# Kernel tuning notes

Measured on AMD Instinct MI355X. Metric: run time of the kernel, lower is better.

## Reference

```python
import jax, jax.numpy as jnp
import numpy as np

B, N, E, IN = 16, 4096, 65536, 128
FILTERS = [256, 256, 128]


def setup_inputs() -> dict:
    key = jax.random.key(0)
    ks = jax.random.split(key, 12)
    inp = {
        "x": jax.random.normal(ks[0], (B, N, IN), dtype=jnp.float32),
        "edge_index": jax.random.randint(ks[1], (B, 2, E), 0, N, dtype=jnp.int32),
        "edge_weight": jax.random.uniform(ks[2], (B, E), dtype=jnp.float32),
        "mask": jax.random.randint(ks[3], (B, N), 0, 2, dtype=jnp.int32),
    }
    dims = [IN] + FILTERS
    for i in range(3):
        inp[f"W{i+1}"] = jax.random.normal(ks[4 + 2 * i], (dims[i], dims[i + 1]), dtype=jnp.float32) / np.sqrt(dims[i]).astype(np.float32)
        inp[f"b{i+1}"] = 0.01 * jax.random.normal(ks[5 + 2 * i], (dims[i + 1],), dtype=jnp.float32)
    return inp


def _gcn_layer(x, ei, ew, valid, W, b):
    # GCNConv(add_self_loops=False, normalize=False):
    #   h = x @ W; out[v] = sum_{(u,v)} ew * h[u]; out += b (valid rows only)
    h = x @ W  # [N, d_out]
    u, v = ei[0], ei[1]
    evalid = valid[u] & valid[v]            # drop edges touching masked-out nodes
    w = jnp.where(evalid, ew, 0.0)
    agg = jnp.zeros_like(h).at[v].add(w[:, None] * h[u])
    return jnp.where(valid[:, None], agg + b, 0.0)


def reference(x, edge_index, edge_weight, mask, W1, b1, W2, b2, W3, b3):
    valid = mask > 0  # [B, N] bool
    out = x
    for W, b in ((W1, b1), (W2, b2), (W3, b3)):
        out = jax.vmap(_gcn_layer, in_axes=(0, 0, 0, 0, None, None))(
            out, edge_index, edge_weight, valid, W, b)
        out = jax.nn.relu(out)  # dropout p=0.0 -> identity
    return out
```

## Files before the change

kernel.cpp:

```cpp
#include <hip/hip_runtime.h>

static constexpr int BATCH = 16;
static constexpr int NNODE = 4096;
static constexpr int NEDGE = 65536;
static constexpr int ROWS  = BATCH * NNODE;
static constexpr int CAP   = 2432;
static constexpr int PM    = BATCH * CAP;
static constexpr int DCAP  = 64;

typedef _Float16 half8  __attribute__((ext_vector_type(8)));
typedef _Float16 half4v __attribute__((ext_vector_type(4)));
typedef _Float16 half2v __attribute__((ext_vector_type(2)));
typedef float    f32x4  __attribute__((ext_vector_type(4)));
typedef float    f32x2  __attribute__((ext_vector_type(2)));

#define GP(p) (const __attribute__((address_space(1))) void*)(p)
#define LP(p) (__attribute__((address_space(3))) void*)(p)

__global__ __launch_bounds__(256) void build_kernel(
    const int* __restrict__ ei, const float* __restrict__ ew,
    const int* __restrict__ mask,
    const float* __restrict__ W1, const float* __restrict__ W2,
    const float* __restrict__ W3,
    int* __restrict__ cursor, unsigned int* __restrict__ bkt,
    _Float16* __restrict__ Wt1, _Float16* __restrict__ Wt2,
    _Float16* __restrict__ Wt3,
    int* __restrict__ vlist, int* __restrict__ validN)
{
    __shared__ int sums[256];
    const int blk = blockIdx.x;
    const int t   = threadIdx.x;

    if (blk < 4096) {
        const int idx = blk * 256 + t;
        const int b = idx >> 16;
        const int e = idx & (NEDGE - 1);
        const int* eib = ei + (size_t)b * 2 * NEDGE;
        const int u = eib[e];
        const int v = eib[NEDGE + e];
        const int mrow = b * NNODE;
        if (mask[mrow + u] != 0 && mask[mrow + v] != 0) {
            const _Float16 w = (_Float16)ew[(size_t)b * NEDGE + e];
            const unsigned short wb = __builtin_bit_cast(unsigned short, w);
            const int pos = atomicAdd(&cursor[mrow + v], 1);
            if (pos < DCAP)
                bkt[(size_t)(mrow + v) * DCAP + pos] = ((unsigned)wb << 16) | (unsigned)u;
        }
    } else if (blk < 4608) {
        const int i = (blk - 4096) * 256 + t;
        if (i < 32768) {
            int k = i >> 8, n = i & 255;
            Wt1[n * 128 + k] = (_Float16)W1[i];
        } else if (i < 98304) {
            int j = i - 32768;
            int k = j >> 8, n = j & 255;
            Wt2[n * 256 + k] = (_Float16)W2[j];
        } else {
            int j = i - 98304;
            int k = j >> 7, n = j & 127;
            Wt3[n * 256 + k] = (_Float16)W3[j];
        }
    } else {
        const int b = blk - 4608;
        const int* mb = mask + b * NNODE;
        for (int i = t; i < CAP; i += 256) vlist[b * CAP + i] = 0;

        int loc[16]; int s = 0;
        #pragma unroll
        for (int i = 0; i < 16; ++i) { loc[i] = (mb[t * 16 + i] != 0); s += loc[i]; }
        sums[t] = s;
        __syncthreads();
        for (int off = 1; off < 256; off <<= 1) {
            int v = (t >= off) ? sums[t - off] : 0;
            __syncthreads();
            sums[t] += v;
            __syncthreads();
        }
        int run = (t == 0) ? 0 : sums[t - 1];
        #pragma unroll
        for (int i = 0; i < 16; ++i) {
            const int n = t * 16 + i;
            if (loc[i]) {
                if (run < CAP) vlist[b * CAP + run] = n;
                ++run;
            }
        }
        if (t == 255) validN[b] = run;
    }
}


__global__ __launch_bounds__(256) void gather_x(
    const int* __restrict__ cursor, const unsigned int* __restrict__ bkt,
    const float* __restrict__ X,
    const int* __restrict__ vlist, const int* __restrict__ validN,
    _Float16* __restrict__ AggX)
{
    constexpr int NU = CAP / 4;
    const int lane = threadIdx.x & 63;
    const int wave = threadIdx.x >> 6;
    const int xcd  = blockIdx.x & 7;
    const int jj   = blockIdx.x >> 3;
    const int batch = 2 * xcd + (jj >= NU);
    const int unit  = (jj >= NU) ? jj - NU : jj;

    const int j = unit * 4 + wave;
    if (j >= validN[batch]) return;
    const int mrow = batch * NNODE;
    const int v = vlist[batch * CAP + j];
    int deg = cursor[mrow + v];
    deg = deg > DCAP ? DCAP : deg;
    const unsigned* bk = bkt + (size_t)(mrow + v) * DCAP;
    const float* Xb = X + (size_t)mrow * 128 + lane * 2;

    float a0 = 0.0f, a1 = 0.0f;
    for (int i = 0; i < deg; i += 8) {
        const int cnt = deg - i;
        unsigned pk[8];
        #pragma unroll
        for (int t = 0; t < 8; ++t) pk[t] = bk[i + t];
        float wj[8]; float2 xv[8];
        #pragma unroll
        for (int t = 0; t < 8; ++t) {
            const bool ok = (t < cnt);
            const unsigned u = pk[t] & 0xFFFu;
            wj[t] = ok ? (float)__builtin_bit_cast(_Float16, (unsigned short)(pk[t] >> 16)) : 0.0f;
            xv[t] = *(const float2*)(Xb + (size_t)u * 128);
        }
        #pragma unroll
        for (int t = 0; t < 8; ++t) { a0 += wj[t] * xv[t].x; a1 += wj[t] * xv[t].y; }
    }
    half2v o = {(_Float16)a0, (_Float16)a1};
    *(half2v*)&AggX[(size_t)(batch * CAP + j) * 128 + lane * 2] = o;
}

__global__ __launch_bounds__(256) void gather_agg(
    const int* __restrict__ cursor, const unsigned int* __restrict__ bkt,
    const _Float16* __restrict__ Ac,
    const int* __restrict__ vlist, const int* __restrict__ validN,
    _Float16* __restrict__ AggA)
{
    constexpr int NU = CAP / 4;
    const int lane = threadIdx.x & 63;
    const int wave = threadIdx.x >> 6;
    const int xcd  = blockIdx.x & 7;
    const int jj   = blockIdx.x >> 3;
    const int batch = 2 * xcd + (jj >= NU);
    const int unit  = (jj >= NU) ? jj - NU : jj;

    const int j = unit * 4 + wave;
    if (j >= validN[batch]) return;
    const int mrow = batch * NNODE;
    const int v = vlist[batch * CAP + j];
    int deg = cursor[mrow + v];
    deg = deg > DCAP ? DCAP : deg;
    const unsigned* bk = bkt + (size_t)(mrow + v) * DCAP;
    const _Float16* Ab = Ac + (size_t)mrow * 256 + lane * 4;

    float a0 = 0.0f, a1 = 0.0f, a2 = 0.0f, a3 = 0.0f;
    for (int i = 0; i < deg; i += 8) {
        const int cnt = deg - i;
        unsigned pk[8];
        #pragma unroll
        for (int t = 0; t < 8; ++t) pk[t] = bk[i + t];
        float wj[8]; half4v hv[8];
        #pragma unroll
        for (int t = 0; t < 8; ++t) {
            const bool ok = (t < cnt);
            const unsigned u = pk[t] & 0xFFFu;
            wj[t] = ok ? (float)__builtin_bit_cast(_Float16, (unsigned short)(pk[t] >> 16)) : 0.0f;
            hv[t] = *(const half4v*)(Ab + (size_t)u * 256);
        }
        #pragma unroll
        for (int t = 0; t < 8; ++t) {
            a0 += wj[t] * (float)hv[t][0];
            a1 += wj[t] * (float)hv[t][1];
            a2 += wj[t] * (float)hv[t][2];
            a3 += wj[t] * (float)hv[t][3];
        }
    }
    half4v o = {(_Float16)a0, (_Float16)a1, (_Float16)a2, (_Float16)a3};
    *(half4v*)&AggA[(size_t)(batch * CAP + j) * 256 + lane * 4] = o;
}

__global__ __launch_bounds__(256, 3) void gemm1_kernel(
    const _Float16* __restrict__ Xc,
    const int* __restrict__ vlist, const int* __restrict__ validN,
    const _Float16* __restrict__ Wt,
    const float* __restrict__ bias,
    _Float16* __restrict__ Ac)
{
    constexpr int K = 128, NW = 64, NI = 4, RST = 72;
    constexpr int NPAN = 4;
    constexpr int NCH  = CAP / 64;
    constexpr int ASZ  = (NPAN * 2048) > (4 * 16 * RST) ? (NPAN * 2048) : (4 * 16 * RST);
    __shared__ _Float16 A16[ASZ];
    __shared__ int s_v[64];

    const int tid  = threadIdx.x;
    const int lane = tid & 63;
    const int wave = tid >> 6;
    const int quad = lane >> 4;
    const int l15  = lane & 15;

    const int xcd  = blockIdx.x & 7;
    const int j    = blockIdx.x >> 3;
    const int batch = 2 * xcd + (j >= NCH);
    const int tile  = (j >= NCH) ? j - NCH : j;
    const int vN   = validN[batch];
    if (tile * 64 >= vN) return;
    const int mrow = batch * NNODE;
    const size_t bm = (size_t)batch * CAP + (size_t)tile * 64;

    if (tid < 64) {
        const int slot = tile * 64 + tid;
        s_v[tid] = (slot < vN) ? vlist[batch * CAP + slot] : 0;
    }
    const int srow = tid >> 2;
    const int sch  = (tid & 3) * 8;
    #pragma unroll
    for (int pp = 0; pp < NPAN; ++pp)
        __builtin_amdgcn_global_load_lds(
            GP(Xc + (bm + srow) * K + pp * 32 + sch),
            LP(A16 + pp * 2048 + tid * 8), 16, 0, 0);
    __syncthreads();

    f32x4 acc[4][NI];
    #pragma unroll
    for (int mi = 0; mi < 4; ++mi)
        #pragma unroll
        for (int ni = 0; ni < NI; ++ni) acc[mi][ni] = (f32x4)0.0f;

    const _Float16* ap = A16 + l15 * 32 + quad * 8;
    const _Float16* wp = Wt + (size_t)(wave * NW + l15) * K + quad * 8;

    #pragma unroll
    for (int pp = 0; pp < NPAN; ++pp) {
        half8 af[4], bf[NI];
        #pragma unroll
        for (int mi = 0; mi < 4; ++mi)
            af[mi] = *(const half8*)(ap + pp * 2048 + mi * 16 * 32);
        #pragma unroll
        for (int ni = 0; ni < NI; ++ni)
            bf[ni] = *(const half8*)(wp + (size_t)ni * 16 * K + pp * 32);
        #pragma unroll
        for (int mi = 0; mi < 4; ++mi)
            #pragma unroll
            for (int ni = 0; ni < NI; ++ni)
                acc[mi][ni] = __builtin_amdgcn_mfma_f32_16x16x32_f16(
                    bf[ni], af[mi], acc[mi][ni], 0, 0, 0);
    }
    __syncthreads();

    _Float16* stg = A16 + wave * 16 * RST;
    const int rr = lane >> 2;
    const int c0 = lane & 3;
    #pragma unroll
    for (int mi = 0; mi < 4; ++mi) {
        #pragma unroll
        for (int ni = 0; ni < NI; ++ni) {
            f32x4 v = acc[mi][ni];
            const f32x4 bv = *(const f32x4*)&bias[wave * NW + ni * 16 + quad * 4];
            half4v o;
            #pragma unroll
            for (int r = 0; r < 4; ++r) o[r] = (_Float16)fmaxf(v[r] + bv[r], 0.0f);
            *(half4v*)&stg[l15 * RST + ni * 16 + quad * 4] = o;
        }
        const int slot = tile * 64 + mi * 16 + rr;
        if (slot < vN) {
            const int vs = s_v[mi * 16 + rr];
            _Float16* hp2 = &Ac[((size_t)mrow + vs) * 256 + wave * NW];
            #pragma unroll
            for (int c = 0; c < NI / 2; ++c) {
                const int ch = (c0 + 4 * c) * 8;
                half8 v = *(const half8*)&stg[rr * RST + ch];
                *(half8*)(hp2 + ch) = v;
            }
        }
    }
}

__global__ __launch_bounds__(256, 3) void gemm23_kernel(
    const _Float16* __restrict__ Xc,
    const int* __restrict__ vlist, const int* __restrict__ validN,
    const _Float16* __restrict__ Wt2,
    const _Float16* __restrict__ Wt3,
    const float* __restrict__ b2,
    _Float16* __restrict__ H3)
{
    constexpr int K    = 256;
    constexpr int NPAN = 8;
    constexpr int NCH  = CAP / 64;
    __shared__ _Float16 A16[NPAN * 2048];
    __shared__ int s_v[64];

    const int tid  = threadIdx.x;
    const int lane = tid & 63;
    const int wave = tid >> 6;
    const int quad = lane >> 4;
    const int l15  = lane & 15;

    const int xcd  = blockIdx.x & 7;
    const int j    = blockIdx.x >> 3;
    const int batch = 2 * xcd + (j >= NCH);
    const int tile  = (j >= NCH) ? j - NCH : j;
    const int vN   = validN[batch];
    if (tile * 64 >= vN) return;
    const int mrow = batch * NNODE;
    const size_t bm = (size_t)batch * CAP + (size_t)tile * 64;

    if (tid < 64) {
        const int slot = tile * 64 + tid;
        s_v[tid] = (slot < vN) ? vlist[batch * CAP + slot] : 0;
    }
    const int srow = tid >> 2;
    const int sch  = (tid & 3) * 8;
    #pragma unroll
    for (int pp = 0; pp < NPAN; ++pp)
        __builtin_amdgcn_global_load_lds(
            GP(Xc + (bm + srow) * K + pp * 32 + sch),
            LP(A16 + pp * 2048 + tid * 8), 16, 0, 0);
    __syncthreads();

    f32x4 acc[4][4];
    #pragma unroll
    for (int mi = 0; mi < 4; ++mi)
        #pragma unroll
        for (int ni = 0; ni < 4; ++ni) acc[mi][ni] = (f32x4)0.0f;

    const _Float16* ap = A16 + l15 * 32 + quad * 8;
    const _Float16* wp = Wt2 + (size_t)(wave * 64 + l15) * K + quad * 8;

    #pragma unroll
    for (int pp = 0; pp < NPAN; ++pp) {
        half8 af[4], bf[4];
        #pragma unroll
        for (int mi = 0; mi < 4; ++mi)
            af[mi] = *(const half8*)(ap + pp * 2048 + mi * 16 * 32);
        #pragma unroll
        for (int ni = 0; ni < 4; ++ni)
            bf[ni] = *(const half8*)(wp + (size_t)ni * 16 * K + pp * 32);
        #pragma unroll
        for (int mi = 0; mi < 4; ++mi)
            #pragma unroll
            for (int ni = 0; ni < 4; ++ni)
                acc[mi][ni] = __builtin_amdgcn_mfma_f32_16x16x32_f16(
                    bf[ni], af[mi], acc[mi][ni], 0, 0, 0);
    }
    __syncthreads();

    #pragma unroll
    for (int mi = 0; mi < 4; ++mi) {
        const int row = mi * 16 + l15;
        #pragma unroll
        for (int ni = 0; ni < 4; ++ni) {
            const int col = wave * 64 + ni * 16 + quad * 4;
            const f32x4 bv = *(const f32x4*)&b2[col];
            f32x4 v = acc[mi][ni];
            half4v o;
            #pragma unroll
            for (int r = 0; r < 4; ++r) o[r] = (_Float16)fmaxf(v[r] + bv[r], 0.0f);
            *(half4v*)&A16[(col >> 5) * 2048 + row * 32 + (col & 31)] = o;
        }
    }
    __syncthreads();

    f32x4 acc2[4][2];
    #pragma unroll
    for (int mi = 0; mi < 4; ++mi)
        #pragma unroll
        for (int ni = 0; ni < 2; ++ni) acc2[mi][ni] = (f32x4)0.0f;

    const _Float16* wp3 = Wt3 + (size_t)(wave * 32 + l15) * K + quad * 8;
    #pragma unroll
    for (int pp = 0; pp < NPAN; ++pp) {
        half8 af[4], bf[2];
        #pragma unroll
        for (int mi = 0; mi < 4; ++mi)
            af[mi] = *(const half8*)(ap + pp * 2048 + mi * 16 * 32);
        #pragma unroll
        for (int ni = 0; ni < 2; ++ni)
            bf[ni] = *(const half8*)(wp3 + (size_t)ni * 16 * K + pp * 32);
        #pragma unroll
        for (int mi = 0; mi < 4; ++mi)
            #pragma unroll
            for (int ni = 0; ni < 2; ++ni)
                acc2[mi][ni] = __builtin_amdgcn_mfma_f32_16x16x32_f16(
                    bf[ni], af[mi], acc2[mi][ni], 0, 0, 0);
    }
    __syncthreads();

    constexpr int RST = 40;
    _Float16* stg = A16 + wave * 16 * RST;
    const int rr = lane >> 2;
    const int c0 = lane & 3;
    #pragma unroll
    for (int mi = 0; mi < 4; ++mi) {
        #pragma unroll
        for (int ni = 0; ni < 2; ++ni) {
            f32x4 v = acc2[mi][ni];
            half4v o;
            #pragma unroll
            for (int r = 0; r < 4; ++r) o[r] = (_Float16)v[r];
            *(half4v*)&stg[l15 * RST + ni * 16 + quad * 4] = o;
        }
        const int slot = tile * 64 + mi * 16 + rr;
        if (slot < vN) {
            const int vs = s_v[mi * 16 + rr];
            _Float16* hp2 = &H3[((size_t)mrow + vs) * 128 + wave * 32];
            const int ch = c0 * 8;
            half8 v = *(const half8*)&stg[rr * RST + ch];
            *(half8*)(hp2 + ch) = v;
        }
    }
}

__global__ __launch_bounds__(256) void gather_final(
    const int* __restrict__ cursor, const unsigned int* __restrict__ bkt,
    const _Float16* __restrict__ H3,
    const int* __restrict__ mask, const float* __restrict__ bias,
    float* __restrict__ OUT)
{
    constexpr int NU = NNODE / 4;
    const int lane = threadIdx.x & 63;
    const int wave = threadIdx.x >> 6;

    const int xcd  = blockIdx.x & 7;
    const int jj   = blockIdx.x >> 3;
    const int batch = 2 * xcd + (jj >= NU);
    const int unit  = (jj >= NU) ? jj - NU : jj;

    const int n = unit * 4 + wave;
    const int mrow = batch * NNODE + n;

    float acc[2] = {};
    if (mask[mrow] != 0) {
        int deg = cursor[mrow];
        deg = deg > DCAP ? DCAP : deg;
        const unsigned* bk = bkt + (size_t)mrow * DCAP;
        const _Float16* Hb = H3 + (size_t)batch * NNODE * 128 + lane * 2;

        for (int i = 0; i < deg; i += 8) {
            const int cnt = deg - i;
            unsigned pk[8];
            #pragma unroll
            for (int t = 0; t < 8; ++t) pk[t] = bk[i + t];
            float wj[8]; const _Float16* hp[8];
            #pragma unroll
            for (int t = 0; t < 8; ++t) {
                const bool ok = (t < cnt);
                const unsigned u = pk[t] & 0xFFFu;
                wj[t] = ok ? (float)__builtin_bit_cast(_Float16, (unsigned short)(pk[t] >> 16)) : 0.0f;
                hp[t] = Hb + (size_t)u * 128;
            }
            half2v hv[8];
            #pragma unroll
            for (int t = 0; t < 8; ++t) hv[t] = *(const half2v*)hp[t];
            #pragma unroll
            for (int t = 0; t < 8; ++t)
                #pragma unroll
                for (int c = 0; c < 2; ++c) acc[c] += wj[t] * (float)hv[t][c];
        }
        #pragma unroll
        for (int c = 0; c < 2; ++c)
            acc[c] = fmaxf(acc[c] + bias[lane * 2 + c], 0.0f);
    }
    f32x2 o = {acc[0], acc[1]};
    *(f32x2*)&OUT[(size_t)mrow * 128 + lane * 2] = o;
}

extern "C" void kernel_launch(void* const* d_in, const int* in_sizes, int n_in,
                              void* d_out, int out_size, void* d_ws, size_t ws_size,
                              hipStream_t stream) {
    const float* x    = (const float*)d_in[0];
    const int*   ei   = (const int*)  d_in[1];
    const float* ew   = (const float*)d_in[2];
    const int*   mask = (const int*)  d_in[3];
    const float* W1   = (const float*)d_in[4];
    const float* b1   = (const float*)d_in[5];
    const float* W2   = (const float*)d_in[6];
    const float* b2   = (const float*)d_in[7];
    const float* W3   = (const float*)d_in[8];
    const float* b3   = (const float*)d_in[9];
    float* out = (float*)d_out;

    char* ws = (char*)d_ws;
    _Float16* Ac   = (_Float16*)(ws);
    _Float16* H3   = (_Float16*)(ws + (32u << 20));
    unsigned int* bkt = (unsigned int*)(ws + (48u << 20));
    _Float16* AggX = (_Float16*)(ws + (64u << 20));
    _Float16* AggA = (_Float16*)(ws + (74u << 20));
    _Float16* Wt1  = (_Float16*)(ws + (94u << 20));
    _Float16* Wt2  = Wt1 + 128 * 256;
    _Float16* Wt3  = Wt2 + 256 * 256;
    int* cursor    = (int*)(Wt3 + 256 * 128);
    int* vlist     = cursor + ROWS;
    int* validN    = vlist + PM;

    const dim3 blk(256);

    hipMemsetAsync(cursor, 0, (size_t)ROWS * sizeof(int), stream);

    build_kernel<<<4624, blk, 0, stream>>>(ei, ew, mask, W1, W2, W3,
                                           cursor, bkt, Wt1, Wt2, Wt3,
                                           vlist, validN);

    const int gemmBlocks = PM / 64;
    const int aggBlocks  = PM / 4;
    const int finBlocks  = ROWS / 4;

    gather_x<<<aggBlocks, blk, 0, stream>>>(cursor, bkt, x, vlist, validN, AggX);
    gemm1_kernel<<<gemmBlocks, blk, 0, stream>>>(AggX, vlist, validN, Wt1, b1, Ac);

    gather_agg<<<aggBlocks, blk, 0, stream>>>(cursor, bkt, Ac, vlist, validN, AggA);
    gemm23_kernel<<<gemmBlocks, blk, 0, stream>>>(AggA, vlist, validN, Wt2, Wt3, b2, H3);

    gather_final<<<finBlocks, blk, 0, stream>>>(cursor, bkt, H3, mask, b3, out);
}
```

Baseline: 208.4 us.

## Fuse memset, build and gather_x into one cooperative kernel with grid syncs

Replaces the cursor memset, the bucket/weight/vlist build kernel and the first gather with a single cooperative kernel of 2048 blocks that uses grid.sync between phases and grid-strided loops over the original virtual block counts. The goal is to remove two kernel launches and the gaps between them. In exchange it adds grid-wide barrier costs, and occupancy is capped by the cooperative grid size. If the cooperative launch fails, it falls back to the old three-launch path.

```diff
diff --git a/kernel.cpp b/kernel.cpp
--- a/kernel.cpp
+++ b/kernel.cpp
@@ -1,4 +1,6 @@
 #include <hip/hip_runtime.h>
+#include <hip/hip_cooperative_groups.h>
+namespace cg = cooperative_groups;
 
 static constexpr int BATCH = 16;
 static constexpr int NNODE = 4096;
@@ -7,6 +9,7 @@
 static constexpr int CAP   = 2432;
 static constexpr int PM    = BATCH * CAP;
 static constexpr int DCAP  = 64;
+static constexpr int GRID_B = 2048;
 
 typedef _Float16 half8  __attribute__((ext_vector_type(8)));
 typedef _Float16 half4v __attribute__((ext_vector_type(4)));
@@ -16,6 +19,128 @@
 
 #define GP(p) (const __attribute__((address_space(1))) void*)(p)
 #define LP(p) (__attribute__((address_space(3))) void*)(p)
+
+__global__ __launch_bounds__(256, 8) void coop_build(
+    const int* __restrict__ ei, const float* __restrict__ ew,
+    const int* __restrict__ mask, const float* __restrict__ X,
+    const float* __restrict__ W1, const float* __restrict__ W2,
+    const float* __restrict__ W3,
+    int* __restrict__ cursor, unsigned int* __restrict__ bkt,
+    _Float16* __restrict__ Wt1, _Float16* __restrict__ Wt2,
+    _Float16* __restrict__ Wt3,
+    int* __restrict__ vlist, int* __restrict__ validN,
+    _Float16* __restrict__ AggX)
+{
+    cg::grid_group grid = cg::this_grid();
+    __shared__ int sums[256];
+    const int tid  = threadIdx.x;
+    const int bx   = blockIdx.x;
+    const int lane = tid & 63;
+    const int wave = tid >> 6;
+
+    {
+        const int i = bx * 256 + tid;
+        if (i < ROWS) cursor[i] = 0;
+    }
+    grid.sync();
+
+    for (int vb = bx; vb < 4624; vb += GRID_B) {
+        if (vb < 4096) {
+            const int idx = vb * 256 + tid;
+            const int b = idx >> 16;
+            const int e = idx & (NEDGE - 1);
+            const int* eib = ei + (size_t)b * 2 * NEDGE;
+            const int u = eib[e];
+            const int v = eib[NEDGE + e];
+            const int mrow = b * NNODE;
+            if (mask[mrow + u] != 0 && mask[mrow + v] != 0) {
+                const _Float16 w = (_Float16)ew[(size_t)b * NEDGE + e];
+                const unsigned short wb = __builtin_bit_cast(unsigned short, w);
+                const int pos = atomicAdd(&cursor[mrow + v], 1);
+                if (pos < DCAP)
+                    bkt[(size_t)(mrow + v) * DCAP + pos] = ((unsigned)wb << 16) | (unsigned)u;
+            }
+        } else if (vb < 4608) {
+            const int i = (vb - 4096) * 256 + tid;
+            if (i < 32768) {
+                int k = i >> 8, n = i & 255;
+                Wt1[n * 128 + k] = (_Float16)W1[i];
+            } else if (i < 98304) {
+                int j = i - 32768;
+                int k = j >> 8, n = j & 255;
+                Wt2[n * 256 + k] = (_Float16)W2[j];
+            } else {
+                int j = i - 98304;
+                int k = j >> 7, n = j & 127;
+                Wt3[n * 256 + k] = (_Float16)W3[j];
+            }
+        } else {
+            const int b = vb - 4608;
+            const int* mb = mask + b * NNODE;
+            for (int i = tid; i < CAP; i += 256) vlist[b * CAP + i] = 0;
+
+            int loc[16]; int s = 0;
+            #pragma unroll
+            for (int i = 0; i < 16; ++i) { loc[i] = (mb[tid * 16 + i] != 0); s += loc[i]; }
+            sums[tid] = s;
+            __syncthreads();
+            for (int off = 1; off < 256; off <<= 1) {
+                int v = (tid >= off) ? sums[tid - off] : 0;
+                __syncthreads();
+                sums[tid] += v;
+                __syncthreads();
+            }
+            int run = (tid == 0) ? 0 : sums[tid - 1];
+            #pragma unroll
+            for (int i = 0; i < 16; ++i) {
+                const int n = tid * 16 + i;
+                if (loc[i]) {
+                    if (run < CAP) vlist[b * CAP + run] = n;
+                    ++run;
+                }
+            }
+            if (tid == 255) validN[b] = run;
+        }
+    }
+    grid.sync();
+
+    for (int vb = bx; vb < 9728; vb += GRID_B) {
+        constexpr int NU = CAP / 4;
+        const int xcd  = vb & 7;
+        const int jj   = vb >> 3;
+        const int batch = 2 * xcd + (jj >= NU);
+        const int unit  = (jj >= NU) ? jj - NU : jj;
+        const int j = unit * 4 + wave;
+        if (j >= validN[batch]) continue;
+        const int mrow = batch * NNODE;
+        const int v = vlist[batch * CAP + j];
+        int deg = cursor[mrow + v];
+        deg = deg > DCAP ? DCAP : deg;
+        const unsigned* bk = bkt + (size_t)(mrow + v) * DCAP;
+        const float* Xb = X + (size_t)mrow * 128 + lane * 2;
+
+        float a0 = 0.0f, a1 = 0.0f;
+        for (int i = 0; i < deg; i += 8) {
+            const int cnt = deg - i;
+            unsigned pk[8];
+            #pragma unroll
+            for (int t = 0; t < 8; ++t) pk[t] = bk[i + t];
+            float wj[8]; float2 xv[8];
+            #pragma unroll
+            for (int t = 0; t < 8; ++t) {
+                const bool ok = (t < cnt);
+                const unsigned u = pk[t] & 0xFFFu;
+                wj[t] = ok ? (float)__builtin_bit_cast(_Float16, (unsigned short)(pk[t] >> 16)) : 0.0f;
+                xv[t] = *(const float2*)(Xb + (size_t)u * 128);
+            }
+            #pragma unroll
+            for (int t = 0; t < 8; ++t) { a0 += wj[t] * xv[t].x; a1 += wj[t] * xv[t].y; }
+        }
+        half2v o = {(_Float16)a0, (_Float16)a1};
+        *(half2v*)&AggX[(size_t)(batch * CAP + j) * 128 + lane * 2] = o;
+    }
+}
+
 
 __global__ __launch_bounds__(256) void build_kernel(
     const int* __restrict__ ei, const float* __restrict__ ew,
@@ -89,12 +214,10 @@
     }
 }
 
-
 __global__ __launch_bounds__(256) void gather_x(
     const int* __restrict__ cursor, const unsigned int* __restrict__ bkt,
-    const float* __restrict__ X,
-    const int* __restrict__ vlist, const int* __restrict__ validN,
-    _Float16* __restrict__ AggX)
+    const float* __restrict__ X, const int* __restrict__ vlist,
+    const int* __restrict__ validN, _Float16* __restrict__ AggX)
 {
     constexpr int NU = CAP / 4;
     const int lane = threadIdx.x & 63;
@@ -136,9 +259,8 @@
 
 __global__ __launch_bounds__(256) void gather_agg(
     const int* __restrict__ cursor, const unsigned int* __restrict__ bkt,
-    const _Float16* __restrict__ Ac,
-    const int* __restrict__ vlist, const int* __restrict__ validN,
-    _Float16* __restrict__ AggA)
+    const _Float16* __restrict__ Ac, const int* __restrict__ vlist,
+    const int* __restrict__ validN, _Float16* __restrict__ AggA)
 {
     constexpr int NU = CAP / 4;
     const int lane = threadIdx.x & 63;
@@ -184,11 +306,9 @@
 }
 
 __global__ __launch_bounds__(256, 3) void gemm1_kernel(
-    const _Float16* __restrict__ Xc,
-    const int* __restrict__ vlist, const int* __restrict__ validN,
-    const _Float16* __restrict__ Wt,
-    const float* __restrict__ bias,
-    _Float16* __restrict__ Ac)
+    const _Float16* __restrict__ Xc, const int* __restrict__ vlist,
+    const int* __restrict__ validN, const _Float16* __restrict__ Wt,
+    const float* __restrict__ bias, _Float16* __restrict__ Ac)
 {
     constexpr int K = 128, NW = 64, NI = 4, RST = 72;
     constexpr int NPAN = 4;
@@ -281,11 +401,9 @@
 }
 
 __global__ __launch_bounds__(256, 3) void gemm23_kernel(
-    const _Float16* __restrict__ Xc,
-    const int* __restrict__ vlist, const int* __restrict__ validN,
-    const _Float16* __restrict__ Wt2,
-    const _Float16* __restrict__ Wt3,
-    const float* __restrict__ b2,
+    const _Float16* __restrict__ Xc, const int* __restrict__ vlist,
+    const int* __restrict__ validN, const _Float16* __restrict__ Wt2,
+    const _Float16* __restrict__ Wt3, const float* __restrict__ b2,
     _Float16* __restrict__ H3)
 {
     constexpr int K    = 256;
@@ -417,9 +535,8 @@
 
 __global__ __launch_bounds__(256) void gather_final(
     const int* __restrict__ cursor, const unsigned int* __restrict__ bkt,
-    const _Float16* __restrict__ H3,
-    const int* __restrict__ mask, const float* __restrict__ bias,
-    float* __restrict__ OUT)
+    const _Float16* __restrict__ H3, const int* __restrict__ mask,
+    const float* __restrict__ bias, float* __restrict__ OUT)
 {
     constexpr int NU = NNODE / 4;
     const int lane = threadIdx.x & 63;
@@ -498,22 +615,27 @@
     int* validN    = vlist + PM;
 
     const dim3 blk(256);
-
-    hipMemsetAsync(cursor, 0, (size_t)ROWS * sizeof(int), stream);
-
-    build_kernel<<<4624, blk, 0, stream>>>(ei, ew, mask, W1, W2, W3,
-                                           cursor, bkt, Wt1, Wt2, Wt3,
-                                           vlist, validN);
-
     const int gemmBlocks = PM / 64;
     const int aggBlocks  = PM / 4;
     const int finBlocks  = ROWS / 4;
 
-    gather_x<<<aggBlocks, blk, 0, stream>>>(cursor, bkt, x, vlist, validN, AggX);
+    void* args[] = {
+        (void*)&ei, (void*)&ew, (void*)&mask, (void*)&x,
+        (void*)&W1, (void*)&W2, (void*)&W3,
+        (void*)&cursor, (void*)&bkt, (void*)&Wt1, (void*)&Wt2, (void*)&Wt3,
+        (void*)&vlist, (void*)&validN, (void*)&AggX };
+    hipError_t err = hipLaunchCooperativeKernel(
+        reinterpret_cast<void*>(coop_build), dim3(GRID_B), blk, args, 0, stream);
+    if (err != hipSuccess) {
+        hipMemsetAsync(cursor, 0, (size_t)ROWS * sizeof(int), stream);
+        build_kernel<<<4624, blk, 0, stream>>>(ei, ew, mask, W1, W2, W3,
+                                               cursor, bkt, Wt1, Wt2, Wt3,
+                                               vlist, validN);
+        gather_x<<<aggBlocks, blk, 0, stream>>>(cursor, bkt, x, vlist, validN, AggX);
+    }
+
     gemm1_kernel<<<gemmBlocks, blk, 0, stream>>>(AggX, vlist, validN, Wt1, b1, Ac);
-
     gather_agg<<<aggBlocks, blk, 0, stream>>>(cursor, bkt, Ac, vlist, validN, AggA);
     gemm23_kernel<<<gemmBlocks, blk, 0, stream>>>(AggA, vlist, validN, Wt2, Wt3, b2, H3);
-
     gather_final<<<finBlocks, blk, 0, stream>>>(cursor, bkt, H3, mask, b3, out);
 }
```

After: 520.8 us. 2.5x slower.
